# Optimization experiments

Hardware: AMD Instinct MI355X
Metric: run time of the kernel (lower is better)

## Reference

```python
import jax, jax.numpy as jnp
import numpy as np

BN_EPS = 1e-5


def _sparse(x, idx, W, b):
    # x: [B, N], idx: [N, K] int, W: [N, K], b: [N]
    # out[b, j] = sum_k x[b, idx[j, k]] * W[j, k] + b[j]
    g = jnp.take(x, idx, axis=1)            # [B, N, K]
    return jnp.einsum('bjk,jk->bj', g, W) + b


def _bn_train(x, gamma, beta):
    # BatchNorm1d in training mode: batch stats, biased variance
    m = jnp.mean(x, axis=0)
    v = jnp.mean(jnp.square(x - m), axis=0)
    return gamma * (x - m) * jax.lax.rsqrt(v + BN_EPS) + beta


def setup_inputs() -> dict:
    key = jax.random.key(0)
    ks = jax.random.split(key, 12)
    B, N = 16384, 784
    s = 0.5  # modest weight scale to keep the deep reuse-chain numerically tame
    return {
        'x':    jax.random.normal(ks[0], (B, N), dtype=jnp.float32),
        'idx1': jax.random.randint(ks[1], (N, 2), 0, N, dtype=jnp.int32),
        'W1':   jax.random.normal(ks[2], (N, 2), dtype=jnp.float32) * s,
        'b1':   jax.random.normal(ks[3], (N,), dtype=jnp.float32) * 0.1,
        'idx2': jax.random.randint(ks[4], (N, 4), 0, N, dtype=jnp.int32),
        'W2':   jax.random.normal(ks[5], (N, 4), dtype=jnp.float32) * s,
        'b2':   jax.random.normal(ks[6], (N,), dtype=jnp.float32) * 0.1,
        'idx3': jax.random.randint(ks[7], (N, 8), 0, N, dtype=jnp.int32),
        'W3':   jax.random.normal(ks[8], (N, 8), dtype=jnp.float32) * s,
        'b3':   jax.random.normal(ks[9], (N,), dtype=jnp.float32) * 0.1,
        'g2':   jnp.ones((N,), dtype=jnp.float32),
        'be2':  jnp.zeros((N,), dtype=jnp.float32),
        'g3':   jnp.ones((N,), dtype=jnp.float32),
        'be3':  jnp.zeros((N,), dtype=jnp.float32),
    }


def reference(x, idx1, W1, b1, idx2, W2, b2, idx3, W3, b3, g2, be2, g3, be3):
    gelu = lambda h: jax.nn.gelu(h, approximate=False)  # torch nn.GELU default (exact)
    h = gelu(_sparse(x, idx1, W1, b1))                  # sp1 -> gelu
    h = _bn_train(gelu(_sparse(h, idx2, W2, b2)), g2, be2)   # sp2 -> gelu -> bn2
    h = _bn_train(gelu(_sparse(h, idx3, W3, b3)), g3, be3)   # sp3 -> gelu -> bn3
    h = _bn_train(gelu(_sparse(h, idx2, W2, b2)), g2, be2)   # sp2 (reused) -> gelu -> bn2
    h = jax.nn.relu(_sparse(h, idx1, W1, b1))                # sp1 (reused) -> relu
    return h
```

## Files before the change

kernel.cpp:

```cpp
#include <hip/hip_runtime.h>
#include <math.h>

static constexpr int BROWS   = 16384;
static constexpr int NC      = 784;
static constexpr int TR      = 16;
static constexpr int THREADS = 512;
static constexpr int NREP    = 4;
static constexpr float EPS   = 1e-5f;
static constexpr float INV_B = 1.0f / (float)BROWS;

#if defined(__has_builtin)
#if __has_builtin(__builtin_amdgcn_global_load_lds)
#define HAVE_ASYNC_LDS 1
#endif
#if __has_builtin(__builtin_amdgcn_rcpf)
#define HAVE_RCPF 1
#endif
#endif

__device__ __forceinline__ void stage16(const float4* g, float4* l) {
#ifdef HAVE_ASYNC_LDS
    __builtin_amdgcn_global_load_lds(
        (const __attribute__((address_space(1))) void*)g,
        (__attribute__((address_space(3))) void*)l, 16, 0, 0);
#else
    *l = *g;
#endif
}

__device__ __forceinline__ float b2f(unsigned short h) {
    union { unsigned u; float f; } v; v.u = ((unsigned)h) << 16; return v.f;
}
__device__ __forceinline__ unsigned short f2b(float f) {
    union { float f; unsigned u; } v; v.f = f;
    const unsigned r = v.u + 0x7fffu + ((v.u >> 16) & 1u);
    return (unsigned short)(r >> 16);
}
__device__ __forceinline__ unsigned pack2(float lo, float hi) {
    return (unsigned)f2b(lo) | ((unsigned)f2b(hi) << 16);
}

__device__ __forceinline__ float fast_rcp(float x) {
#ifdef HAVE_RCPF
    return __builtin_amdgcn_rcpf(x);
#else
    return 1.0f / x;
#endif
}

__device__ __forceinline__ float gelu_f(float x) {
    const float a = fabsf(x) * 0.7071067811865475f;
    const float t = fast_rcp(fmaf(0.3275911f, a, 1.0f));
    float p = fmaf(t, 1.061405429f, -1.453152027f);
    p = fmaf(t, p, 1.421413741f);
    p = fmaf(t, p, -0.284496736f);
    p = fmaf(t, p, 0.254829592f);
    p *= t;
    const float e  = __expf(-a * a);
    const float er = fmaf(-p, e, 1.0f);
    return 0.5f * x * (1.0f + copysignf(er, x));
}

__global__ __launch_bounds__(THREADS, 6)
void layer12(const float* __restrict__ x,
             const int* __restrict__ idx1, const float* __restrict__ W1, const float* __restrict__ b1,
             const int* __restrict__ idx2, const float* __restrict__ W2, const float* __restrict__ b2,
             unsigned short* __restrict__ u2, float* __restrict__ ssum, float* __restrict__ ssq)
{
    __shared__ __align__(16) unsigned short rows[TR * NC];
    const int tid  = threadIdx.x;
    const int row0 = blockIdx.x * TR;

    {
        const float4* x4 = (const float4*)(x + (size_t)row0 * NC);
        uint2* r2 = (uint2*)rows;
        for (int i = tid; i < TR * NC / 4; i += THREADS) {
            const float4 v = x4[i];
            uint2 pk; pk.x = pack2(v.x, v.y); pk.y = pack2(v.z, v.w);
            r2[i] = pk;
        }
    }
    __syncthreads();

    for (int s = 0; s < TR; s += 8) {
        float h[2][8];
        #pragma unroll
        for (int g = 0; g < 2; ++g) {
            const int j = tid + g * THREADS;
            if (j < NC) {
                const int   i0 = idx1[2 * j], i1 = idx1[2 * j + 1];
                const float w0 = W1[2 * j],   w1 = W1[2 * j + 1], bb = b1[j];
                #pragma unroll
                for (int r = 0; r < 8; ++r) {
                    const float acc = fmaf(b2f(rows[(s + r) * NC + i0]), w0,
                                      fmaf(b2f(rows[(s + r) * NC + i1]), w1, bb));
                    h[g][r] = gelu_f(acc);
                }
            }
        }
        __syncthreads();
        #pragma unroll
        for (int g = 0; g < 2; ++g) {
            const int j = tid + g * THREADS;
            if (j < NC)
                #pragma unroll
                for (int r = 0; r < 8; ++r) rows[(s + r) * NC + j] = f2b(h[g][r]);
        }
        __syncthreads();
    }

    #pragma unroll
    for (int g = 0; g < 2; ++g) {
        const int j = tid + g * THREADS;
        if (j < NC) {
            int ji[4]; float jw[4];
            #pragma unroll
            for (int k = 0; k < 4; ++k) { ji[k] = idx2[4 * j + k]; jw[k] = W2[4 * j + k]; }
            const float jb = b2[j];
            float s1 = 0.0f, s2 = 0.0f;
            #pragma unroll 4
            for (int r = 0; r < TR; ++r) {
                float acc = jb;
                #pragma unroll
                for (int k = 0; k < 4; ++k) acc = fmaf(b2f(rows[r * NC + ji[k]]), jw[k], acc);
                const float u = gelu_f(acc);
                u2[(size_t)(row0 + r) * NC + j] = f2b(u);
                s1 += u; s2 = fmaf(u, u, s2);
            }
            const int rep = blockIdx.x & (NREP - 1);
            atomicAdd(&ssum[rep * NC + j], s1);
            atomicAdd(&ssq[rep * NC + j],  s2);
        }
    }
}

template<int K, bool FINAL>
__global__ __launch_bounds__(THREADS, 6)
void layer_bn(const unsigned short* __restrict__ in,
              const int* __restrict__ idx, const float* __restrict__ W, const float* __restrict__ bias,
              const float* __restrict__ gamma, const float* __restrict__ beta,
              const float* __restrict__ psum,  const float* __restrict__ psq,
              void* __restrict__ outv, float* __restrict__ ssum, float* __restrict__ ssq)
{
    __shared__ __align__(16) unsigned short rows[TR * NC];
    __shared__ float s_sc[NC], s_sh[NC];
    const int tid  = threadIdx.x;
    const int row0 = blockIdx.x * TR;

    {
        const float4* src = (const float4*)(in + (size_t)row0 * NC);
        float4*       dst = (float4*)rows;
        for (int i = tid; i < TR * NC * 2 / 16; i += THREADS) stage16(src + i, dst + i);
    }
    for (int j = tid; j < NC; j += THREADS) {
        float s1 = 0.0f, s2 = 0.0f;
        #pragma unroll
        for (int r = 0; r < NREP; ++r) { s1 += psum[r * NC + j]; s2 += psq[r * NC + j]; }
        const float m   = s1 * INV_B;
        const float var = fmaf(-m, m, s2 * INV_B);
        const float sc  = gamma[j] * rsqrtf(var + EPS);
        s_sc[j] = sc;
        s_sh[j] = fmaf(-m, sc, beta[j]);
    }
    __syncthreads();

    #pragma unroll
    for (int g = 0; g < 2; ++g) {
        const int j = tid + g * THREADS;
        if (j < NC) {
            int ji[K]; float jw[K];
            float jb = bias[j];
            #pragma unroll
            for (int k = 0; k < K; ++k) {
                const int   c = idx[K * j + k];
                const float w = W[K * j + k];
                ji[k] = c;
                jw[k] = w * s_sc[c];
                jb    = fmaf(w, s_sh[c], jb);
            }
            float s1 = 0.0f, s2 = 0.0f;
            #pragma unroll 4
            for (int r = 0; r < TR; ++r) {
                float acc = jb;
                #pragma unroll
                for (int k = 0; k < K; ++k) acc = fmaf(b2f(rows[r * NC + ji[k]]), jw[k], acc);
                if (FINAL) {
                    ((float*)outv)[(size_t)(row0 + r) * NC + j] = fmaxf(acc, 0.0f);
                } else {
                    const float u = gelu_f(acc);
                    ((unsigned short*)outv)[(size_t)(row0 + r) * NC + j] = f2b(u);
                    s1 += u; s2 = fmaf(u, u, s2);
                }
            }
            if (!FINAL) {
                const int rep = blockIdx.x & (NREP - 1);
                atomicAdd(&ssum[rep * NC + j], s1);
                atomicAdd(&ssq[rep * NC + j],  s2);
            }
        }
    }
}

extern "C" void kernel_launch(void* const* d_in, const int* in_sizes, int n_in,
                              void* d_out, int out_size, void* d_ws, size_t ws_size,
                              hipStream_t stream)
{
    const float* x    = (const float*)d_in[0];
    const int*   idx1 = (const int*)  d_in[1];
    const float* W1   = (const float*)d_in[2];
    const float* b1   = (const float*)d_in[3];
    const int*   idx2 = (const int*)  d_in[4];
    const float* W2   = (const float*)d_in[5];
    const float* b2   = (const float*)d_in[6];
    const int*   idx3 = (const int*)  d_in[7];
    const float* W3   = (const float*)d_in[8];
    const float* b3   = (const float*)d_in[9];
    const float* g2   = (const float*)d_in[10];
    const float* be2  = (const float*)d_in[11];
    const float* g3   = (const float*)d_in[12];
    const float* be3  = (const float*)d_in[13];
    float* out = (float*)d_out;

    const size_t BN_ELEMS = (size_t)BROWS * NC;
    unsigned short* ws0 = (unsigned short*)d_ws;
    unsigned short* ws1 = ws0 + BN_ELEMS;
    float* p = (float*)(ws1 + BN_ELEMS);
    float* sum2a = p; p += NREP * NC;  float* ssq2a = p; p += NREP * NC;
    float* sum3  = p; p += NREP * NC;  float* ssq3  = p; p += NREP * NC;
    float* sum2b = p; p += NREP * NC;  float* ssq2b = p; p += NREP * NC;

    hipMemsetAsync(sum2a, 0, 6 * NREP * NC * sizeof(float), stream);

    const dim3 grid(BROWS / TR), blk(THREADS);

    layer12<<<grid, blk, 0, stream>>>(x, idx1, W1, b1, idx2, W2, b2, ws0, sum2a, ssq2a);
    layer_bn<8, false><<<grid, blk, 0, stream>>>(
        ws0, idx3, W3, b3, g2, be2, sum2a, ssq2a, ws1, sum3, ssq3);
    layer_bn<4, false><<<grid, blk, 0, stream>>>(
        ws1, idx2, W2, b2, g3, be3, sum3, ssq3, ws0, sum2b, ssq2b);
    layer_bn<2, true><<<grid, blk, 0, stream>>>(
        ws0, idx1, W1, b1, g2, be2, sum2b, ssq2b, out, nullptr, nullptr);
}
```

Before: 205.8 us.

## Pack four rows per column into 64-bit bf16 quads for gathers

Intermediate activations are now stored row-interleaved: each 64-bit word holds the bf16 values of four consecutive rows for one column, both in LDS and in the global workspace. A single LDS gather then fetches four rows' worth of data, cutting the number of random-index LDS reads by four and making global stores 8 bytes wide. The first kernel now reads x column-wise with strided loads to build the quads, which may coalesce worse. Launch bounds are also raised to 8 waves per EU, which may increase register pressure or cause spills.

```diff
diff --git a/kernel.cpp b/kernel.cpp
--- a/kernel.cpp
+++ b/kernel.cpp
@@ -3,8 +3,10 @@
 
 static constexpr int BROWS   = 16384;
 static constexpr int NC      = 784;
-static constexpr int TR      = 16;
+static constexpr int TRB     = 16;
 static constexpr int THREADS = 512;
+static constexpr int NBLK    = BROWS / TRB;
+static constexpr int NSLOT   = 2;
 static constexpr int NREP    = 4;
 static constexpr float EPS   = 1e-5f;
 static constexpr float INV_B = 1.0f / (float)BROWS;
@@ -28,9 +30,6 @@
 #endif
 }
 
-__device__ __forceinline__ float b2f(unsigned short h) {
-    union { unsigned u; float f; } v; v.u = ((unsigned)h) << 16; return v.f;
-}
 __device__ __forceinline__ unsigned short f2b(float f) {
     union { float f; unsigned u; } v; v.f = f;
     const unsigned r = v.u + 0x7fffu + ((v.u >> 16) & 1u);
@@ -38,6 +37,15 @@
 }
 __device__ __forceinline__ unsigned pack2(float lo, float hi) {
     return (unsigned)f2b(lo) | ((unsigned)f2b(hi) << 16);
+}
+__device__ __forceinline__ unsigned long long pack4(float a, float b, float c, float d) {
+    return (unsigned long long)pack2(a, b) | ((unsigned long long)pack2(c, d) << 32);
+}
+__device__ __forceinline__ void unpack4(unsigned long long v, float f[4]) {
+    const unsigned lo = (unsigned)v, hi = (unsigned)(v >> 32);
+    union { unsigned u; float f; } a, b, c, d;
+    a.u = lo << 16; b.u = lo & 0xffff0000u; c.u = hi << 16; d.u = hi & 0xffff0000u;
+    f[0] = a.f; f[1] = b.f; f[2] = c.f; f[3] = d.f;
 }
 
 __device__ __forceinline__ float fast_rcp(float x) {
@@ -61,71 +69,86 @@
     return 0.5f * x * (1.0f + copysignf(er, x));
 }
 
-__global__ __launch_bounds__(THREADS, 6)
+__global__ __launch_bounds__(THREADS, 8)
 void layer12(const float* __restrict__ x,
              const int* __restrict__ idx1, const float* __restrict__ W1, const float* __restrict__ b1,
              const int* __restrict__ idx2, const float* __restrict__ W2, const float* __restrict__ b2,
-             unsigned short* __restrict__ u2, float* __restrict__ ssum, float* __restrict__ ssq)
+             unsigned long long* __restrict__ uq2,
+             float* __restrict__ ssum, float* __restrict__ ssq)
 {
-    __shared__ __align__(16) unsigned short rows[TR * NC];
+    __shared__ unsigned long long quad[4 * NC];
     const int tid  = threadIdx.x;
-    const int row0 = blockIdx.x * TR;
-
-    {
-        const float4* x4 = (const float4*)(x + (size_t)row0 * NC);
-        uint2* r2 = (uint2*)rows;
-        for (int i = tid; i < TR * NC / 4; i += THREADS) {
-            const float4 v = x4[i];
-            uint2 pk; pk.x = pack2(v.x, v.y); pk.y = pack2(v.z, v.w);
-            r2[i] = pk;
+    const int row0 = blockIdx.x * TRB;
+
+    #pragma unroll
+    for (int slot = 0; slot < NSLOT; ++slot) {
+        const int c = tid + slot * THREADS;
+        if (c < NC) {
+            #pragma unroll
+            for (int q = 0; q < 4; ++q) {
+                const size_t base = (size_t)(row0 + 4 * q) * NC + c;
+                quad[q * NC + c] = pack4(x[base], x[base + NC], x[base + 2 * NC], x[base + 3 * NC]);
+            }
         }
     }
     __syncthreads();
 
-    for (int s = 0; s < TR; s += 8) {
-        float h[2][8];
+    for (int half = 0; half < 2; ++half) {
+        float h[NSLOT][8];
         #pragma unroll
-        for (int g = 0; g < 2; ++g) {
-            const int j = tid + g * THREADS;
+        for (int slot = 0; slot < NSLOT; ++slot) {
+            const int j = tid + slot * THREADS;
             if (j < NC) {
                 const int   i0 = idx1[2 * j], i1 = idx1[2 * j + 1];
                 const float w0 = W1[2 * j],   w1 = W1[2 * j + 1], bb = b1[j];
                 #pragma unroll
-                for (int r = 0; r < 8; ++r) {
-                    const float acc = fmaf(b2f(rows[(s + r) * NC + i0]), w0,
-                                      fmaf(b2f(rows[(s + r) * NC + i1]), w1, bb));
-                    h[g][r] = gelu_f(acc);
+                for (int qq = 0; qq < 2; ++qq) {
+                    float f0[4], f1[4];
+                    unpack4(quad[(2 * half + qq) * NC + i0], f0);
+                    unpack4(quad[(2 * half + qq) * NC + i1], f1);
+                    #pragma unroll
+                    for (int rr = 0; rr < 4; ++rr)
+                        h[slot][4 * qq + rr] = gelu_f(fmaf(f0[rr], w0, fmaf(f1[rr], w1, bb)));
                 }
             }
         }
         __syncthreads();
         #pragma unroll
-        for (int g = 0; g < 2; ++g) {
-            const int j = tid + g * THREADS;
-            if (j < NC)
-                #pragma unroll
-                for (int r = 0; r < 8; ++r) rows[(s + r) * NC + j] = f2b(h[g][r]);
+        for (int slot = 0; slot < NSLOT; ++slot) {
+            const int j = tid + slot * THREADS;
+            if (j < NC) {
+                quad[(2 * half + 0) * NC + j] = pack4(h[slot][0], h[slot][1], h[slot][2], h[slot][3]);
+                quad[(2 * half + 1) * NC + j] = pack4(h[slot][4], h[slot][5], h[slot][6], h[slot][7]);
+            }
         }
         __syncthreads();
     }
 
-    #pragma unroll
-    for (int g = 0; g < 2; ++g) {
-        const int j = tid + g * THREADS;
+    for (int slot = 0; slot < NSLOT; ++slot) {
+        const int j = tid + slot * THREADS;
         if (j < NC) {
             int ji[4]; float jw[4];
             #pragma unroll
             for (int k = 0; k < 4; ++k) { ji[k] = idx2[4 * j + k]; jw[k] = W2[4 * j + k]; }
             const float jb = b2[j];
             float s1 = 0.0f, s2 = 0.0f;
-            #pragma unroll 4
-            for (int r = 0; r < TR; ++r) {
-                float acc = jb;
-                #pragma unroll
-                for (int k = 0; k < 4; ++k) acc = fmaf(b2f(rows[r * NC + ji[k]]), jw[k], acc);
-                const float u = gelu_f(acc);
-                u2[(size_t)(row0 + r) * NC + j] = f2b(u);
-                s1 += u; s2 = fmaf(u, u, s2);
+            #pragma unroll
+            for (int q = 0; q < 4; ++q) {
+                float acc[4] = { jb, jb, jb, jb };
+                #pragma unroll
+                for (int k = 0; k < 4; ++k) {
+                    float f[4];
+                    unpack4(quad[q * NC + ji[k]], f);
+                    #pragma unroll
+                    for (int rr = 0; rr < 4; ++rr) acc[rr] = fmaf(f[rr], jw[k], acc[rr]);
+                }
+                float u[4];
+                #pragma unroll
+                for (int rr = 0; rr < 4; ++rr) {
+                    u[rr] = gelu_f(acc[rr]);
+                    s1 += u[rr]; s2 = fmaf(u[rr], u[rr], s2);
+                }
+                uq2[(size_t)(blockIdx.x * 4 + q) * NC + j] = pack4(u[0], u[1], u[2], u[3]);
             }
             const int rep = blockIdx.x & (NREP - 1);
             atomicAdd(&ssum[rep * NC + j], s1);
@@ -135,22 +158,23 @@
 }
 
 template<int K, bool FINAL>
-__global__ __launch_bounds__(THREADS, 6)
-void layer_bn(const unsigned short* __restrict__ in,
+__global__ __launch_bounds__(THREADS, 8)
+void layer_bn(const unsigned long long* __restrict__ uqin,
               const int* __restrict__ idx, const float* __restrict__ W, const float* __restrict__ bias,
               const float* __restrict__ gamma, const float* __restrict__ beta,
-              const float* __restrict__ psum,  const float* __restrict__ psq,
-              void* __restrict__ outv, float* __restrict__ ssum, float* __restrict__ ssq)
+              const float* __restrict__ psum, const float* __restrict__ psq,
+              unsigned long long* __restrict__ uqout, float* __restrict__ fout,
+              float* __restrict__ ssum, float* __restrict__ ssq)
 {
-    __shared__ __align__(16) unsigned short rows[TR * NC];
+    __shared__ unsigned long long quad[4 * NC];
     __shared__ float s_sc[NC], s_sh[NC];
     const int tid  = threadIdx.x;
-    const int row0 = blockIdx.x * TR;
+    const int row0 = blockIdx.x * TRB;
 
     {
-        const float4* src = (const float4*)(in + (size_t)row0 * NC);
-        float4*       dst = (float4*)rows;
-        for (int i = tid; i < TR * NC * 2 / 16; i += THREADS) stage16(src + i, dst + i);
+        const float4* src = (const float4*)(uqin + (size_t)blockIdx.x * 4 * NC);
+        float4*       dst = (float4*)quad;
+        for (int i = tid; i < 4 * NC / 2; i += THREADS) stage16(src + i, dst + i);
     }
     for (int j = tid; j < NC; j += THREADS) {
         float s1 = 0.0f, s2 = 0.0f;
@@ -164,9 +188,8 @@
     }
     __syncthreads();
 
-    #pragma unroll
-    for (int g = 0; g < 2; ++g) {
-        const int j = tid + g * THREADS;
+    for (int slot = 0; slot < NSLOT; ++slot) {
+        const int j = tid + slot * THREADS;
         if (j < NC) {
             int ji[K]; float jw[K];
             float jb = bias[j];
@@ -174,22 +197,31 @@
             for (int k = 0; k < K; ++k) {
                 const int   c = idx[K * j + k];
                 const float w = W[K * j + k];
-                ji[k] = c;
-                jw[k] = w * s_sc[c];
-                jb    = fmaf(w, s_sh[c], jb);
+                ji[k] = c; jw[k] = w * s_sc[c]; jb = fmaf(w, s_sh[c], jb);
             }
             float s1 = 0.0f, s2 = 0.0f;
-            #pragma unroll 4
-            for (int r = 0; r < TR; ++r) {
-                float acc = jb;
-                #pragma unroll
-                for (int k = 0; k < K; ++k) acc = fmaf(b2f(rows[r * NC + ji[k]]), jw[k], acc);
+            #pragma unroll
+            for (int q = 0; q < 4; ++q) {
+                float acc[4] = { jb, jb, jb, jb };
+                #pragma unroll
+                for (int k = 0; k < K; ++k) {
+                    float f[4];
+                    unpack4(quad[q * NC + ji[k]], f);
+                    #pragma unroll
+                    for (int rr = 0; rr < 4; ++rr) acc[rr] = fmaf(f[rr], jw[k], acc[rr]);
+                }
                 if (FINAL) {
-                    ((float*)outv)[(size_t)(row0 + r) * NC + j] = fmaxf(acc, 0.0f);
+                    #pragma unroll
+                    for (int rr = 0; rr < 4; ++rr)
+                        fout[(size_t)(row0 + 4 * q + rr) * NC + j] = fmaxf(acc[rr], 0.0f);
                 } else {
-                    const float u = gelu_f(acc);
-                    ((unsigned short*)outv)[(size_t)(row0 + r) * NC + j] = f2b(u);
-                    s1 += u; s2 = fmaf(u, u, s2);
+                    float u[4];
+                    #pragma unroll
+                    for (int rr = 0; rr < 4; ++rr) {
+                        u[rr] = gelu_f(acc[rr]);
+                        s1 += u[rr]; s2 = fmaf(u[rr], u[rr], s2);
+                    }
+                    uqout[(size_t)(blockIdx.x * 4 + q) * NC + j] = pack4(u[0], u[1], u[2], u[3]);
                 }
             }
             if (!FINAL) {
@@ -221,23 +253,23 @@
     const float* be3  = (const float*)d_in[13];
     float* out = (float*)d_out;
 
-    const size_t BN_ELEMS = (size_t)BROWS * NC;
-    unsigned short* ws0 = (unsigned short*)d_ws;
-    unsigned short* ws1 = ws0 + BN_ELEMS;
-    float* p = (float*)(ws1 + BN_ELEMS);
+    const size_t QN = (size_t)NBLK * 4 * NC;
+    unsigned long long* ws0 = (unsigned long long*)d_ws;
+    unsigned long long* ws1 = ws0 + QN;
+    float* p = (float*)(ws1 + QN);
     float* sum2a = p; p += NREP * NC;  float* ssq2a = p; p += NREP * NC;
     float* sum3  = p; p += NREP * NC;  float* ssq3  = p; p += NREP * NC;
     float* sum2b = p; p += NREP * NC;  float* ssq2b = p; p += NREP * NC;
 
     hipMemsetAsync(sum2a, 0, 6 * NREP * NC * sizeof(float), stream);
 
-    const dim3 grid(BROWS / TR), blk(THREADS);
+    const dim3 grid(NBLK), blk(THREADS);
 
     layer12<<<grid, blk, 0, stream>>>(x, idx1, W1, b1, idx2, W2, b2, ws0, sum2a, ssq2a);
     layer_bn<8, false><<<grid, blk, 0, stream>>>(
-        ws0, idx3, W3, b3, g2, be2, sum2a, ssq2a, ws1, sum3, ssq3);
+        ws0, idx3, W3, b3, g2, be2, sum2a, ssq2a, ws1, nullptr, sum3, ssq3);
     layer_bn<4, false><<<grid, blk, 0, stream>>>(
-        ws1, idx2, W2, b2, g3, be3, sum3, ssq3, ws0, sum2b, ssq2b);
+        ws1, idx2, W2, b2, g3, be3, sum3, ssq3, ws0, nullptr, sum2b, ssq2b);
     layer_bn<2, true><<<grid, blk, 0, stream>>>(
-        ws0, idx1, W1, b1, g2, be2, sum2b, ssq2b, out, nullptr, nullptr);
-}
+        ws0, idx1, W1, b1, g2, be2, sum2b, ssq2b, nullptr, out, nullptr, nullptr);
+}
```

After: 192.6 us. -6.5%, faster.
